# Performance work log

Measured on AMD Instinct MI355X. Metric: run time of the kernel, lower is better.

The kernel has to match this reference:

```python
import jax, jax.numpy as jnp
import numpy as np

N = 50000      # nodes
E = 800000     # edges (before self-loops)
F_IN = 256     # num_features
H = 8          # heads (conv1)
C = 32         # hidden_size per head (conv1)
OUT = 2        # conv2 out channels (1 head)
NEG_SLOPE = 0.2


def setup_inputs() -> dict:
    key = jax.random.key(0)
    ks = jax.random.split(key, 12)
    x = jax.random.normal(ks[0], (N, F_IN), jnp.float32)
    edge_index = jax.random.randint(ks[1], (2, E), 0, N, dtype=jnp.int64)

    def glorot(k, shape):
        fan = shape[0] if len(shape) == 2 else int(np.prod(shape))
        s = float(np.sqrt(6.0 / (fan + shape[-1])))
        return jax.random.uniform(k, shape, jnp.float32, -s, s)

    W1 = glorot(ks[2], (F_IN, H * C))
    att_src1 = glorot(ks[3], (H, C))
    att_dst1 = glorot(ks[4], (H, C))
    b1 = jnp.zeros((H * C,), jnp.float32)
    W2 = glorot(ks[5], (H * C, 1 * OUT))
    att_src2 = glorot(ks[6], (1, OUT))
    att_dst2 = glorot(ks[7], (1, OUT))
    b2 = jnp.zeros((OUT,), jnp.float32)
    return {"x": x, "edge_index": edge_index, "W1": W1, "att_src1": att_src1,
            "att_dst1": att_dst1, "b1": b1, "W2": W2, "att_src2": att_src2,
            "att_dst2": att_dst2, "b2": b2}


def gat_conv(x, src, dst, W, a_src, a_dst, b, heads, ch, n):
    # x: [n, f] -> projected [n, heads, ch]
    xp = (x @ W).reshape(n, heads, ch)
    alpha_src = jnp.einsum('nhc,hc->nh', xp, a_src)   # [n, H]
    alpha_dst = jnp.einsum('nhc,hc->nh', xp, a_dst)   # [n, H]
    e = jax.nn.leaky_relu(alpha_src[src] + alpha_dst[dst], NEG_SLOPE)  # [E', H]
    # segment softmax over edges grouped by destination node
    m = jax.ops.segment_max(e, dst, num_segments=n)                    # [n, H]
    p = jnp.exp(e - m[dst])
    denom = jax.ops.segment_sum(p, dst, num_segments=n)                # [n, H]
    alpha = p / denom[dst]                                             # [E', H]
    # weighted scatter-aggregate of source messages
    out = jax.ops.segment_sum(xp[src] * alpha[:, :, None], dst, num_segments=n)
    return out.reshape(n, heads * ch) + b


def reference(x, edge_index, W1, att_src1, att_dst1, b1, W2, att_src2, att_dst2, b2):
    n = x.shape[0]
    loops = jnp.arange(n, dtype=edge_index.dtype)  # GATConv add_self_loops=True
    src = jnp.concatenate([edge_index[0], loops])
    dst = jnp.concatenate([edge_index[1], loops])
    h = jax.nn.relu(gat_conv(x, src, dst, W1, att_src1, att_dst1, b1, H, C, n))
    # eval mode: F.dropout and attention dropout are identity
    return gat_conv(h, src, dst, W2, att_src2, att_dst2, b2, 1, OUT, n)
```

## Files before the change

kernel.cpp:

```cpp
#include <hip/hip_runtime.h>
#include <math.h>

#define N_NODES 50000
#define N_EDGES 800000
#define EP (N_EDGES + N_NODES)
#define NEG 0.2f
#define SCAN_BLOCKS 49

typedef __attribute__((ext_vector_type(8))) short bf16x8;
typedef __attribute__((ext_vector_type(4))) float f32x4;
typedef __attribute__((ext_vector_type(2))) float f32x2;

static __device__ __forceinline__ unsigned short bf16_rn(float f) {
    union { float f; unsigned int u; } v; v.f = f;
    unsigned int u = v.u;
    unsigned int r = (u + 0x7FFFu + ((u >> 16) & 1u)) >> 16;
    return (unsigned short)r;
}
static __device__ __forceinline__ float bf16_tof(unsigned short u) {
    union { unsigned int u; float f; } v; v.u = ((unsigned int)u) << 16;
    return v.f;
}
static __device__ __forceinline__ f32x2 bf2_unpack(unsigned int u) {
    union { unsigned int i; float f; } a, b;
    a.i = u << 16; b.i = u & 0xFFFF0000u;
    return (f32x2){a.f, b.f};
}


__global__ void k_hist(const int* __restrict__ ei, int* __restrict__ counts) {
    int e = blockIdx.x * 256 + threadIdx.x;
    if (e >= EP) return;
    int d = (e < N_EDGES) ? ei[N_EDGES + e] : (e - N_EDGES);
    atomicAdd(&counts[d], 1);
}

__global__ void k_scan_block(const int* __restrict__ counts, int* __restrict__ excl,
                             int* __restrict__ bsums) {
    __shared__ int wsum[4];
    int b = blockIdx.x, t = threadIdx.x;
    int lane = t & 63, w = t >> 6;
    int i0 = b * 1024 + t * 4;
    int v0 = (i0 + 0 < N_NODES) ? counts[i0 + 0] : 0;
    int v1 = (i0 + 1 < N_NODES) ? counts[i0 + 1] : 0;
    int v2 = (i0 + 2 < N_NODES) ? counts[i0 + 2] : 0;
    int v3 = (i0 + 3 < N_NODES) ? counts[i0 + 3] : 0;
    int s = v0 + v1 + v2 + v3;
    int incl = s;
    #pragma unroll
    for (int d = 1; d < 64; d <<= 1) {
        int u = __shfl_up(incl, d);
        if (lane >= d) incl += u;
    }
    if (lane == 63) wsum[w] = incl;
    __syncthreads();
    if (t == 0) {
        int run = 0;
        #pragma unroll
        for (int i = 0; i < 4; ++i) { int x = wsum[i]; wsum[i] = run; run += x; }
        bsums[b] = run;
    }
    __syncthreads();
    int base = wsum[w] + incl - s;
    if (i0 + 0 < N_NODES) excl[i0 + 0] = base;
    if (i0 + 1 < N_NODES) excl[i0 + 1] = base + v0;
    if (i0 + 2 < N_NODES) excl[i0 + 2] = base + v0 + v1;
    if (i0 + 3 < N_NODES) excl[i0 + 3] = base + v0 + v1 + v2;
}

__global__ void k_scan_add(int* __restrict__ row_ptr, const int* __restrict__ bsums) {
    __shared__ int soff;
    int b = blockIdx.x, t = threadIdx.x;
    if (t < 64) {
        int v = (t < SCAN_BLOCKS) ? bsums[t] : 0;
        int incl = v;
        #pragma unroll
        for (int d = 1; d < 64; d <<= 1) {
            int u = __shfl_up(incl, d);
            if (t >= d) incl += u;
        }
        if (t == b) soff = incl - v;
    }
    __syncthreads();
    int off = soff;
    int i0 = b * 1024 + t * 4;
    #pragma unroll
    for (int j = 0; j < 4; ++j)
        if (i0 + j < N_NODES) row_ptr[i0 + j] += off;
    if (b == 0 && t == 0) row_ptr[N_NODES] = EP;
}

__global__ void k_scatter(const int* __restrict__ ei, const int* __restrict__ row_ptr,
                          int* __restrict__ fill, int* __restrict__ colb) {
    int e = blockIdx.x * 256 + threadIdx.x;
    if (e >= EP) return;
    int s, d;
    if (e < N_EDGES) { s = ei[e]; d = ei[N_EDGES + e]; }
    else             { s = e - N_EDGES; d = s; }
    int pos = row_ptr[d] + atomicAdd(&fill[d], 1);
    colb[pos] = s;
}

__global__ void k_cvtWfrag(const float* __restrict__ W1, bf16x8* __restrict__ Wfrag) {
    int ft = blockIdx.x * 256 + threadIdx.x;
    int c = ft >> 10, rem = ft & 1023;
    int nt = rem >> 6, l = rem & 63;
    int n = (l & 15) * 16 + nt;
    int k0 = c * 32 + (l >> 4) * 8;
    bf16x8 f;
    #pragma unroll
    for (int j = 0; j < 8; ++j)
        f[j] = (short)bf16_rn(W1[(k0 + j) * 256 + n]);
    Wfrag[ft] = f;
}

#define GM_GRID 782
__global__ __launch_bounds__(256) void
k_gemm1m(const float* __restrict__ x, const bf16x8* __restrict__ Wfrag,
         unsigned short* __restrict__ xp1b,
         const float* __restrict__ asrc, const float* __restrict__ adst,
         float* __restrict__ as1, float* __restrict__ ad1) {
    __shared__ bf16x8 lds[1024];
    int t = threadIdx.x, l = t & 63, w = t >> 6;
    int rowbase = blockIdx.x * 64 + w * 16;
    int m = l & 15, kg = l >> 4;

    f32x4 acc[16];
    #pragma unroll
    for (int nt = 0; nt < 16; ++nt)
        acc[nt] = (f32x4){0.f, 0.f, 0.f, 0.f};

    int r0 = rowbase + m;
    if (r0 > N_NODES - 1) r0 = N_NODES - 1;
    const float4* x4 = (const float4*)x;

    for (int c = 0; c < 8; ++c) {
        __syncthreads();
        const bf16x8* src = Wfrag + c * 1024;
        #pragma unroll
        for (int q = 0; q < 4; ++q)
            lds[q * 256 + t] = src[q * 256 + t];
        __syncthreads();

        int kb = (c * 32 + kg * 8) >> 2;
        float4 xa0 = x4[r0 * 64 + kb], xb0 = x4[r0 * 64 + kb + 1];
        bf16x8 aF0;
        aF0[0] = (short)bf16_rn(xa0.x); aF0[1] = (short)bf16_rn(xa0.y);
        aF0[2] = (short)bf16_rn(xa0.z); aF0[3] = (short)bf16_rn(xa0.w);
        aF0[4] = (short)bf16_rn(xb0.x); aF0[5] = (short)bf16_rn(xb0.y);
        aF0[6] = (short)bf16_rn(xb0.z); aF0[7] = (short)bf16_rn(xb0.w);

        #pragma unroll
        for (int nt = 0; nt < 16; ++nt) {
            bf16x8 bF = lds[nt * 64 + l];
            acc[nt] = __builtin_amdgcn_mfma_f32_16x16x32_bf16(aF0, bF, acc[nt], 0, 0, 0);
        }
    }

    int cbase = l & 15, rq = l >> 4;
    float asV[16], adV[16];
    #pragma unroll
    for (int q = 0; q < 4; ++q) {
        float4 sa = ((const float4*)asrc)[cbase * 4 + q];
        float4 da = ((const float4*)adst)[cbase * 4 + q];
        asV[q * 4 + 0] = sa.x; asV[q * 4 + 1] = sa.y; asV[q * 4 + 2] = sa.z; asV[q * 4 + 3] = sa.w;
        adV[q * 4 + 0] = da.x; adV[q * 4 + 1] = da.y; adV[q * 4 + 2] = da.z; adV[q * 4 + 3] = da.w;
    }
    #pragma unroll
    for (int reg = 0; reg < 4; ++reg) {
        int gr = rowbase + rq * 4 + reg;
        unsigned int ob[8];
        float ps = 0.f, pd = 0.f;
        #pragma unroll
        for (int q = 0; q < 8; ++q) {
            float v0 = acc[2 * q][reg], v1 = acc[2 * q + 1][reg];
            ob[q] = (unsigned int)bf16_rn(v0) | ((unsigned int)bf16_rn(v1) << 16);
            ps = fmaf(v0, asV[2 * q], ps);     ps = fmaf(v1, asV[2 * q + 1], ps);
            pd = fmaf(v0, adV[2 * q], pd);     pd = fmaf(v1, adV[2 * q + 1], pd);
        }
        ps += __shfl_xor(ps, 1);
        pd += __shfl_xor(pd, 1);
        if (gr < N_NODES) {
            uint4* dst = (uint4*)(xp1b + gr * 256 + cbase * 16);
            dst[0] = make_uint4(ob[0], ob[1], ob[2], ob[3]);
            dst[1] = make_uint4(ob[4], ob[5], ob[6], ob[7]);
            if ((l & 1) == 0) {
                as1[gr * 8 + (cbase >> 1)] = ps;
                ad1[gr * 8 + (cbase >> 1)] = pd;
            }
        }
    }
}

__global__ void k_agg1(const ushort4* __restrict__ xpb, const float* __restrict__ as1,
                       const float* __restrict__ ad1, const int* __restrict__ row_ptr,
                       const int* __restrict__ colb, const float* __restrict__ b1,
                       const float* __restrict__ W2, const float* __restrict__ as2w,
                       const float* __restrict__ ad2w,
                       float* __restrict__ xp2, float* __restrict__ as2,
                       float* __restrict__ ad2) {
    int t = threadIdx.x, l = t & 63, w = t >> 6;
    int n = blockIdx.x * 4 + w;
    int hl = l & 31;
    int half = l >> 5;
    int hidx = hl >> 2;
    float adn = ad1[n * 8 + hidx];
    int start = row_ptr[n], end = row_ptr[n + 1];
    const uint4* xp4 = (const uint4*)xpb;
    f32x2 acc0 = {0.f, 0.f}, acc1 = {0.f, 0.f}, acc2 = {0.f, 0.f}, acc3 = {0.f, 0.f};
    float den = 0.f;
    int j = start;
    for (; j + 4 <= end; j += 4) {
        int jj0 = j + half, jj1 = j + 2 + half;
        int s0 = colb[jj0], s1 = colb[jj1];
        uint4 r0 = xp4[s0 * 32 + hl];
        uint4 r1 = xp4[s1 * 32 + hl];
        float e0 = as1[s0 * 8 + hidx] + adn;
        float e1 = as1[s1 * 8 + hidx] + adn;
        e0 = (e0 > 0.f) ? e0 : NEG * e0;
        e1 = (e1 > 0.f) ? e1 : NEG * e1;
        float p0 = __expf(e0), p1 = __expf(e1);
        den += p0 + p1;
        f32x2 q0 = {p0, p0}, q1 = {p1, p1};
        acc0 += q0 * bf2_unpack(r0.x);  acc1 += q0 * bf2_unpack(r0.y);
        acc2 += q0 * bf2_unpack(r0.z);  acc3 += q0 * bf2_unpack(r0.w);
        acc0 += q1 * bf2_unpack(r1.x);  acc1 += q1 * bf2_unpack(r1.y);
        acc2 += q1 * bf2_unpack(r1.z);  acc3 += q1 * bf2_unpack(r1.w);
    }
    for (; j < end; j += 2) {
        int jj = j + half;
        bool v = jj < end;
        int s = colb[v ? jj : start];
        uint4 r = xp4[s * 32 + hl];
        float e = as1[s * 8 + hidx] + adn;
        e = (e > 0.f) ? e : NEG * e;
        float p = v ? __expf(e) : 0.f;
        den += p;
        f32x2 q = {p, p};
        acc0 += q * bf2_unpack(r.x);  acc1 += q * bf2_unpack(r.y);
        acc2 += q * bf2_unpack(r.z);  acc3 += q * bf2_unpack(r.w);
    }
    acc0[0] += __shfl_xor(acc0[0], 32); acc0[1] += __shfl_xor(acc0[1], 32);
    acc1[0] += __shfl_xor(acc1[0], 32); acc1[1] += __shfl_xor(acc1[1], 32);
    acc2[0] += __shfl_xor(acc2[0], 32); acc2[1] += __shfl_xor(acc2[1], 32);
    acc3[0] += __shfl_xor(acc3[0], 32); acc3[1] += __shfl_xor(acc3[1], 32);
    den += __shfl_xor(den, 32);

    float inv = 1.f / den;
    float4 ba = ((const float4*)b1)[hl * 2];
    float4 bb = ((const float4*)b1)[hl * 2 + 1];
    float o0 = fmaxf(acc0[0] * inv + ba.x, 0.f);
    float o1 = fmaxf(acc0[1] * inv + ba.y, 0.f);
    float o2 = fmaxf(acc1[0] * inv + ba.z, 0.f);
    float o3 = fmaxf(acc1[1] * inv + ba.w, 0.f);
    float o4 = fmaxf(acc2[0] * inv + bb.x, 0.f);
    float o5 = fmaxf(acc2[1] * inv + bb.y, 0.f);
    float o6 = fmaxf(acc3[0] * inv + bb.z, 0.f);
    float o7 = fmaxf(acc3[1] * inv + bb.w, 0.f);
    const float4* W4 = (const float4*)W2;
    float4 wa = W4[hl * 4 + 0];
    float4 wb = W4[hl * 4 + 1];
    float4 wc = W4[hl * 4 + 2];
    float4 wd = W4[hl * 4 + 3];
    float d0 = o0 * wa.x + o1 * wa.z + o2 * wb.x + o3 * wb.z
             + o4 * wc.x + o5 * wc.z + o6 * wd.x + o7 * wd.z;
    float d1 = o0 * wa.y + o1 * wa.w + o2 * wb.y + o3 * wb.w
             + o4 * wc.y + o5 * wc.w + o6 * wd.y + o7 * wd.w;
    #pragma unroll
    for (int m = 1; m < 32; m <<= 1) {
        d0 += __shfl_xor(d0, m);
        d1 += __shfl_xor(d1, m);
    }
    if (l == 0) {
        xp2[2 * n] = d0;
        xp2[2 * n + 1] = d1;
        as2[n] = d0 * as2w[0] + d1 * as2w[1];
        ad2[n] = d0 * ad2w[0] + d1 * ad2w[1];
    }
}

__global__ void k_agg2(const float* __restrict__ xp2, const float* __restrict__ as2,
                       const float* __restrict__ ad2, const int* __restrict__ row_ptr,
                       const int* __restrict__ colb, const float* __restrict__ b2,
                       float* __restrict__ out) {
    int t = threadIdx.x;
    int g = t >> 4, lane = t & 15;
    int n = blockIdx.x * 16 + g;
    int start = row_ptr[n], end = row_ptr[n + 1];
    float adn = ad2[n];
    float a0 = 0.f, a1 = 0.f, den = 0.f;
    for (int j = start + lane; j < end; j += 16) {
        int s = colb[j];
        float e = as2[s] + adn;
        e = (e > 0.f) ? e : NEG * e;
        float p = __expf(e);
        den += p;
        float2 xv = ((const float2*)xp2)[s];
        a0 = fmaf(p, xv.x, a0);
        a1 = fmaf(p, xv.y, a1);
    }
    #pragma unroll
    for (int m = 1; m < 16; m <<= 1) {
        a0 += __shfl_xor(a0, m);
        a1 += __shfl_xor(a1, m);
        den += __shfl_xor(den, m);
    }
    if (lane == 0) {
        out[2 * n] = a0 / den + b2[0];
        out[2 * n + 1] = a1 / den + b2[1];
    }
}

extern "C" void kernel_launch(void* const* d_in, const int* in_sizes, int n_in,
                              void* d_out, int out_size, void* d_ws, size_t ws_size,
                              hipStream_t stream) {
    const float* x     = (const float*)d_in[0];
    const int*   ei    = (const int*)d_in[1];
    const float* W1    = (const float*)d_in[2];
    const float* asrc1 = (const float*)d_in[3];
    const float* adst1 = (const float*)d_in[4];
    const float* b1    = (const float*)d_in[5];
    const float* W2    = (const float*)d_in[6];
    const float* asrc2 = (const float*)d_in[7];
    const float* adst2 = (const float*)d_in[8];
    const float* b2    = (const float*)d_in[9];
    float* out = (float*)d_out;

    char* ws = (char*)d_ws;
    unsigned short* xp1b = (unsigned short*)(ws + 0);
    bf16x8* Wfrag  = (bf16x8*)(ws + 25600000);
    float* as1     = (float*)(ws + 102400000);
    float* ad1     = (float*)(ws + 104000000);
    float* xp2     = (float*)(ws + 105600000);
    float* as2     = (float*)(ws + 106000000);
    float* ad2     = (float*)(ws + 106200000);
    int*   counts  = (int*)  (ws + 106400000);
    int*   fill    = (int*)  (ws + 106600000);
    int*   row_ptr = (int*)  (ws + 106800000);
    int*   colb    = (int*)  (ws + 107000064);
    int*   bsums   = (int*)  (ws + 110400064);

    hipMemsetAsync(counts, 0, 400000, stream);

    int egrid = (EP + 255) / 256;
    k_hist      <<<egrid,       256, 0, stream>>>(ei, counts);
    k_scan_block<<<SCAN_BLOCKS, 256, 0, stream>>>(counts, row_ptr, bsums);
    k_scan_add  <<<SCAN_BLOCKS, 256, 0, stream>>>(row_ptr, bsums);
    k_scatter   <<<egrid,       256, 0, stream>>>(ei, row_ptr, fill, colb);

    k_cvtWfrag  <<<32,     256, 0, stream>>>(W1, Wfrag);
    k_gemm1m    <<<GM_GRID, 256, 0, stream>>>(x, Wfrag, xp1b, asrc1, adst1, as1, ad1);
    k_agg1      <<<12500,  256, 0, stream>>>((const ushort4*)xp1b, as1, ad1, row_ptr, colb,
                                             b1, W2, asrc2, adst2, xp2, as2, ad2);
    k_agg2      <<<3125,   256, 0, stream>>>(xp2, as2, ad2, row_ptr, colb, b2, out);
}
```

Measured before the change: 294.1 us.

## Store layer-1 features head-major and aggregate one head per block

The GEMM epilogue now writes projected features and attention scores in head-major layout, so each head's data is a contiguous 64-byte row per node. Aggregation runs one block per (node group, head), with 8 lanes per edge reading 8-byte pieces. Partial layer-2 projections are written per head and reduced in a new small k_post kernel. The goal is better cache locality per head, since each block works on one 3.2MB slice. The cost is reading colb and row_ptr eight times, using narrower gathers, and adding a kernel launch plus an hpart round trip.

```diff
diff --git a/kernel.cpp b/kernel.cpp
--- a/kernel.cpp
+++ b/kernel.cpp
@@ -6,6 +6,7 @@
 #define EP (N_EDGES + N_NODES)
 #define NEG 0.2f
 #define SCAN_BLOCKS 49
+#define HB N_NODES
 
 typedef __attribute__((ext_vector_type(8))) short bf16x8;
 typedef __attribute__((ext_vector_type(4))) float f32x4;
@@ -16,10 +17,6 @@
     unsigned int u = v.u;
     unsigned int r = (u + 0x7FFFu + ((u >> 16) & 1u)) >> 16;
     return (unsigned short)r;
-}
-static __device__ __forceinline__ float bf16_tof(unsigned short u) {
-    union { unsigned int u; float f; } v; v.u = ((unsigned int)u) << 16;
-    return v.f;
 }
 static __device__ __forceinline__ f32x2 bf2_unpack(unsigned int u) {
     union { unsigned int i; float f; } a, b;
@@ -117,9 +114,9 @@
 #define GM_GRID 782
 __global__ __launch_bounds__(256) void
 k_gemm1m(const float* __restrict__ x, const bf16x8* __restrict__ Wfrag,
-         unsigned short* __restrict__ xp1b,
+         unsigned short* __restrict__ xph,
          const float* __restrict__ asrc, const float* __restrict__ adst,
-         float* __restrict__ as1, float* __restrict__ ad1) {
+         float* __restrict__ as1T, float* __restrict__ ad1T) {
     __shared__ bf16x8 lds[1024];
     int t = threadIdx.x, l = t & 63, w = t >> 6;
     int rowbase = blockIdx.x * 64 + w * 16;
@@ -158,6 +155,7 @@
     }
 
     int cbase = l & 15, rq = l >> 4;
+    int head = cbase >> 1, hhalf = cbase & 1;
     float asV[16], adV[16];
     #pragma unroll
     for (int q = 0; q < 4; ++q) {
@@ -181,102 +179,102 @@
         ps += __shfl_xor(ps, 1);
         pd += __shfl_xor(pd, 1);
         if (gr < N_NODES) {
-            uint4* dst = (uint4*)(xp1b + gr * 256 + cbase * 16);
+            uint4* dst = (uint4*)(xph + (head * HB + gr) * 32 + hhalf * 16);
             dst[0] = make_uint4(ob[0], ob[1], ob[2], ob[3]);
             dst[1] = make_uint4(ob[4], ob[5], ob[6], ob[7]);
-            if ((l & 1) == 0) {
-                as1[gr * 8 + (cbase >> 1)] = ps;
-                ad1[gr * 8 + (cbase >> 1)] = pd;
+            if (hhalf == 0) {
+                as1T[head * HB + gr] = ps;
+                ad1T[head * HB + gr] = pd;
             }
         }
     }
 }
 
-__global__ void k_agg1(const ushort4* __restrict__ xpb, const float* __restrict__ as1,
-                       const float* __restrict__ ad1, const int* __restrict__ row_ptr,
-                       const int* __restrict__ colb, const float* __restrict__ b1,
-                       const float* __restrict__ W2, const float* __restrict__ as2w,
-                       const float* __restrict__ ad2w,
-                       float* __restrict__ xp2, float* __restrict__ as2,
-                       float* __restrict__ ad2) {
+__global__ __launch_bounds__(256) void
+k_aggh(const uint2* __restrict__ xph, const float* __restrict__ as1T,
+       const float* __restrict__ ad1T, const int* __restrict__ row_ptr,
+       const int* __restrict__ colb, const float* __restrict__ b1,
+       const float* __restrict__ W2, float2* __restrict__ hpart) {
     int t = threadIdx.x, l = t & 63, w = t >> 6;
-    int n = blockIdx.x * 4 + w;
-    int hl = l & 31;
-    int half = l >> 5;
-    int hidx = hl >> 2;
-    float adn = ad1[n * 8 + hidx];
+    int bid = blockIdx.x;
+    int h = bid & 7;
+    int ng = bid >> 3;
+    int n = ng * 4 + w;
+    int o = l >> 3;
+    int sub = l & 7;
+    float adn = ad1T[h * HB + n];
     int start = row_ptr[n], end = row_ptr[n + 1];
-    const uint4* xp4 = (const uint4*)xpb;
-    f32x2 acc0 = {0.f, 0.f}, acc1 = {0.f, 0.f}, acc2 = {0.f, 0.f}, acc3 = {0.f, 0.f};
+    const float* asb = as1T + h * HB;
+    const uint2* xb = xph + (size_t)h * (HB * 8);
+    f32x2 accA = {0.f, 0.f}, accB = {0.f, 0.f};
     float den = 0.f;
     int j = start;
-    for (; j + 4 <= end; j += 4) {
-        int jj0 = j + half, jj1 = j + 2 + half;
-        int s0 = colb[jj0], s1 = colb[jj1];
-        uint4 r0 = xp4[s0 * 32 + hl];
-        uint4 r1 = xp4[s1 * 32 + hl];
-        float e0 = as1[s0 * 8 + hidx] + adn;
-        float e1 = as1[s1 * 8 + hidx] + adn;
-        e0 = (e0 > 0.f) ? e0 : NEG * e0;
-        e1 = (e1 > 0.f) ? e1 : NEG * e1;
-        float p0 = __expf(e0), p1 = __expf(e1);
-        den += p0 + p1;
-        f32x2 q0 = {p0, p0}, q1 = {p1, p1};
-        acc0 += q0 * bf2_unpack(r0.x);  acc1 += q0 * bf2_unpack(r0.y);
-        acc2 += q0 * bf2_unpack(r0.z);  acc3 += q0 * bf2_unpack(r0.w);
-        acc0 += q1 * bf2_unpack(r1.x);  acc1 += q1 * bf2_unpack(r1.y);
-        acc2 += q1 * bf2_unpack(r1.z);  acc3 += q1 * bf2_unpack(r1.w);
-    }
-    for (; j < end; j += 2) {
-        int jj = j + half;
-        bool v = jj < end;
-        int s = colb[v ? jj : start];
-        uint4 r = xp4[s * 32 + hl];
-        float e = as1[s * 8 + hidx] + adn;
+    for (; j + 8 <= end; j += 8) {
+        int s = colb[j + o];
+        float e = asb[s] + adn;
         e = (e > 0.f) ? e : NEG * e;
-        float p = v ? __expf(e) : 0.f;
+        float p = __expf(e);
         den += p;
+        uint2 r = xb[s * 8 + sub];
         f32x2 q = {p, p};
-        acc0 += q * bf2_unpack(r.x);  acc1 += q * bf2_unpack(r.y);
-        acc2 += q * bf2_unpack(r.z);  acc3 += q * bf2_unpack(r.w);
-    }
-    acc0[0] += __shfl_xor(acc0[0], 32); acc0[1] += __shfl_xor(acc0[1], 32);
-    acc1[0] += __shfl_xor(acc1[0], 32); acc1[1] += __shfl_xor(acc1[1], 32);
-    acc2[0] += __shfl_xor(acc2[0], 32); acc2[1] += __shfl_xor(acc2[1], 32);
-    acc3[0] += __shfl_xor(acc3[0], 32); acc3[1] += __shfl_xor(acc3[1], 32);
-    den += __shfl_xor(den, 32);
-
+        accA += q * bf2_unpack(r.x);
+        accB += q * bf2_unpack(r.y);
+    }
+    if (j + o < end) {
+        int s = colb[j + o];
+        float e = asb[s] + adn;
+        e = (e > 0.f) ? e : NEG * e;
+        float p = __expf(e);
+        den += p;
+        uint2 r = xb[s * 8 + sub];
+        f32x2 q = {p, p};
+        accA += q * bf2_unpack(r.x);
+        accB += q * bf2_unpack(r.y);
+    }
+    #pragma unroll
+    for (int m = 8; m < 64; m <<= 1) {
+        accA[0] += __shfl_xor(accA[0], m);
+        accA[1] += __shfl_xor(accA[1], m);
+        accB[0] += __shfl_xor(accB[0], m);
+        accB[1] += __shfl_xor(accB[1], m);
+        den += __shfl_xor(den, m);
+    }
     float inv = 1.f / den;
-    float4 ba = ((const float4*)b1)[hl * 2];
-    float4 bb = ((const float4*)b1)[hl * 2 + 1];
-    float o0 = fmaxf(acc0[0] * inv + ba.x, 0.f);
-    float o1 = fmaxf(acc0[1] * inv + ba.y, 0.f);
-    float o2 = fmaxf(acc1[0] * inv + ba.z, 0.f);
-    float o3 = fmaxf(acc1[1] * inv + ba.w, 0.f);
-    float o4 = fmaxf(acc2[0] * inv + bb.x, 0.f);
-    float o5 = fmaxf(acc2[1] * inv + bb.y, 0.f);
-    float o6 = fmaxf(acc3[0] * inv + bb.z, 0.f);
-    float o7 = fmaxf(acc3[1] * inv + bb.w, 0.f);
+    float4 bv = ((const float4*)b1)[h * 8 + sub];
+    float o0 = fmaxf(accA[0] * inv + bv.x, 0.f);
+    float o1 = fmaxf(accA[1] * inv + bv.y, 0.f);
+    float o2 = fmaxf(accB[0] * inv + bv.z, 0.f);
+    float o3 = fmaxf(accB[1] * inv + bv.w, 0.f);
     const float4* W4 = (const float4*)W2;
-    float4 wa = W4[hl * 4 + 0];
-    float4 wb = W4[hl * 4 + 1];
-    float4 wc = W4[hl * 4 + 2];
-    float4 wd = W4[hl * 4 + 3];
-    float d0 = o0 * wa.x + o1 * wa.z + o2 * wb.x + o3 * wb.z
-             + o4 * wc.x + o5 * wc.z + o6 * wd.x + o7 * wd.z;
-    float d1 = o0 * wa.y + o1 * wa.w + o2 * wb.y + o3 * wb.w
-             + o4 * wc.y + o5 * wc.w + o6 * wd.y + o7 * wd.w;
-    #pragma unroll
-    for (int m = 1; m < 32; m <<= 1) {
+    float4 wa = W4[h * 16 + sub * 2 + 0];
+    float4 wb = W4[h * 16 + sub * 2 + 1];
+    float d0 = o0 * wa.x + o1 * wa.z + o2 * wb.x + o3 * wb.z;
+    float d1 = o0 * wa.y + o1 * wa.w + o2 * wb.y + o3 * wb.w;
+    #pragma unroll
+    for (int m = 1; m < 8; m <<= 1) {
         d0 += __shfl_xor(d0, m);
         d1 += __shfl_xor(d1, m);
     }
-    if (l == 0) {
-        xp2[2 * n] = d0;
-        xp2[2 * n + 1] = d1;
-        as2[n] = d0 * as2w[0] + d1 * as2w[1];
-        ad2[n] = d0 * ad2w[0] + d1 * ad2w[1];
-    }
+    if (l == 0) hpart[n * 8 + h] = (float2){d0, d1};
+}
+
+__global__ void k_post(const float2* __restrict__ hpart, const float* __restrict__ as2w,
+                       const float* __restrict__ ad2w, float* __restrict__ xp2,
+                       float* __restrict__ as2, float* __restrict__ ad2) {
+    int n = blockIdx.x * 256 + threadIdx.x;
+    if (n >= N_NODES) return;
+    const float4* hp4 = (const float4*)(hpart + n * 8);
+    float d0 = 0.f, d1 = 0.f;
+    #pragma unroll
+    for (int q = 0; q < 4; ++q) {
+        float4 v = hp4[q];
+        d0 += v.x + v.z;
+        d1 += v.y + v.w;
+    }
+    xp2[2 * n] = d0;
+    xp2[2 * n + 1] = d1;
+    as2[n] = d0 * as2w[0] + d1 * as2w[1];
+    ad2[n] = d0 * ad2w[0] + d1 * ad2w[1];
 }
 
 __global__ void k_agg2(const float* __restrict__ xp2, const float* __restrict__ as2,
@@ -327,10 +325,11 @@
     float* out = (float*)d_out;
 
     char* ws = (char*)d_ws;
-    unsigned short* xp1b = (unsigned short*)(ws + 0);
+    unsigned short* xph = (unsigned short*)(ws + 0);
     bf16x8* Wfrag  = (bf16x8*)(ws + 25600000);
-    float* as1     = (float*)(ws + 102400000);
-    float* ad1     = (float*)(ws + 104000000);
+    float2* hpart  = (float2*)(ws + 25800000);
+    float* as1T    = (float*)(ws + 102400000);
+    float* ad1T    = (float*)(ws + 104000000);
     float* xp2     = (float*)(ws + 105600000);
     float* as2     = (float*)(ws + 106000000);
     float* ad2     = (float*)(ws + 106200000);
@@ -349,8 +348,9 @@
     k_scatter   <<<egrid,       256, 0, stream>>>(ei, row_ptr, fill, colb);
 
     k_cvtWfrag  <<<32,     256, 0, stream>>>(W1, Wfrag);
-    k_gemm1m    <<<GM_GRID, 256, 0, stream>>>(x, Wfrag, xp1b, asrc1, adst1, as1, ad1);
-    k_agg1      <<<12500,  256, 0, stream>>>((const ushort4*)xp1b, as1, ad1, row_ptr, colb,
-                                             b1, W2, asrc2, adst2, xp2, as2, ad2);
-    k_agg2      <<<3125,   256, 0, stream>>>(xp2, as2, ad2, row_ptr, colb, b2, out);
-}
+    k_gemm1m   <<<GM_GRID, 256, 0, stream>>>(x, Wfrag, xph, asrc1, adst1, as1T, ad1T);
+    k_aggh     <<<100000,  256, 0, stream>>>((const uint2*)xph, as1T, ad1T, row_ptr, colb,
+                                             b1, W2, hpart);
+    k_post     <<<196,     256, 0, stream>>>(hpart, asrc2, adst2, xp2, as2, ad2);
+    k_agg2     <<<3125,    256, 0, stream>>>(xp2, as2, ad2, row_ptr, colb, b2, out);
+}
```

Measured after the change: 370.9 us. 1.26x slower.
